# Kernel optimization log

Hardware: AMD Instinct MI355X
Metric: run time of the kernel (lower is better)

## Reference

```python
import jax, jax.numpy as jnp
import numpy as np

HIDDEN = 1024
HEADS = 16
HEAD_DIM = HIDDEN // HEADS
ROPE_BASE = 10000.0


def rope_cos_sin(seq_len, head_dim, dtype=jnp.float32):
    inv_freq = 1.0 / (ROPE_BASE ** (jnp.arange(0, head_dim, 2, dtype=jnp.float32) / head_dim))
    t = jnp.arange(seq_len, dtype=jnp.float32)
    freqs = jnp.einsum('i,j->ij', t, inv_freq)          # [L, head_dim/2]
    emb = jnp.concatenate([freqs, freqs], axis=-1)       # [L, head_dim]
    return emb.astype(dtype), jnp.cos(emb).astype(dtype), jnp.sin(emb).astype(dtype)


def rotate_half(x):
    half = x.shape[-1] // 2
    return jnp.concatenate([-x[..., half:], x[..., :half]], axis=-1)


def setup_inputs() -> dict:
    key = jax.random.key(0)
    kx, kq, kk, kv, ko = jax.random.split(key, 5)
    B, L = 4, 2048
    scale = 1.0 / np.sqrt(HIDDEN)
    x = jax.random.normal(kx, (B, L, HIDDEN), dtype=jnp.float32)
    Wq = jax.random.normal(kq, (HIDDEN, HIDDEN), dtype=jnp.float32) * scale
    Wk = jax.random.normal(kk, (HIDDEN, HIDDEN), dtype=jnp.float32) * scale
    Wv = jax.random.normal(kv, (HIDDEN, HIDDEN), dtype=jnp.float32) * scale
    Wo = jax.random.normal(ko, (HIDDEN, HIDDEN), dtype=jnp.float32) * scale
    return {"x": x, "Wq": Wq, "Wk": Wk, "Wv": Wv, "Wo": Wo}


def reference(x, Wq, Wk, Wv, Wo):
    B, L, D = x.shape
    H, Hd = HEADS, HEAD_DIM
    # projections (nn.Linear: y = x @ W.T; weights here stored already as [out,in])
    q = (x @ Wq.T).reshape(B, L, H, Hd).transpose(0, 2, 1, 3)  # [B,H,L,Hd]
    k = (x @ Wk.T).reshape(B, L, H, Hd).transpose(0, 2, 1, 3)
    v = (x @ Wv.T).reshape(B, L, H, Hd).transpose(0, 2, 1, 3)
    _, cos, sin = rope_cos_sin(L, Hd, x.dtype)                  # [L, Hd]
    cos = cos[None, None, :, :]
    sin = sin[None, None, :, :]
    q = q * cos + rotate_half(q) * sin
    k = k * cos + rotate_half(k) * sin
    scores = jnp.einsum('bhqd,bhkd->bhqk', q, k) / np.sqrt(Hd)  # [B,H,L,L]
    attn = jax.nn.softmax(scores, axis=-1)
    out = jnp.einsum('bhqk,bhkd->bhqd', attn, v)                # [B,H,L,Hd]
    out = out.transpose(0, 2, 1, 3).reshape(B, L, D)
    return out @ Wo.T
```

## Files before the change

### kernel.cpp

```cpp
#include <hip/hip_runtime.h>
#include <math.h>

#define BB 4
#define LL 2048
#define DD 1024
#define HH 16
#define HD 64
#define BL (BB*LL)

typedef __attribute__((ext_vector_type(8))) short bf16x8;
typedef __attribute__((ext_vector_type(4))) short bf16x4;
typedef __attribute__((ext_vector_type(4))) float f32x4;

__device__ inline short f2bf(float f) {
    union { float f; unsigned u; } v; v.f = f;
    unsigned r = v.u + 0x7fffu + ((v.u >> 16) & 1u);
    return (short)(r >> 16);
}

__device__ inline unsigned pk_bf16(float a, float b) {
    union { float f; unsigned u; } x, y; x.f = a; y.f = b;
    return (x.u >> 16) | (y.u & 0xffff0000u);
}

__device__ inline float exp2x(float x) {
#if __has_builtin(__builtin_amdgcn_exp2f)
    return __builtin_amdgcn_exp2f(x);
#else
    return exp2f(x);
#endif
}

__device__ inline void gload_lds16(const void* g, void* l) {
    __builtin_amdgcn_global_load_lds(
        (const __attribute__((address_space(1))) unsigned int*)g,
        (__attribute__((address_space(3))) unsigned int*)l, 16, 0, 0);
}

__global__ __launch_bounds__(256) void cast_kernel(
    const float* __restrict__ in, short* __restrict__ out, int n)
{
    int i = (blockIdx.x * 256 + threadIdx.x) * 8;
    float4 a = *(const float4*)(in + i);
    float4 b = *(const float4*)(in + i + 4);
    bf16x8 o;
    o[0]=f2bf(a.x); o[1]=f2bf(a.y); o[2]=f2bf(a.z); o[3]=f2bf(a.w);
    o[4]=f2bf(b.x); o[5]=f2bf(b.y); o[6]=f2bf(b.z); o[7]=f2bf(b.w);
    *(bf16x8*)(out + i) = o;
}

__global__ __launch_bounds__(256) void cast4_kernel(
    const float* __restrict__ w0, const float* __restrict__ w1,
    const float* __restrict__ w2, const float* __restrict__ w3,
    short* __restrict__ out)
{
    const int nw_blocks = (DD*DD) / 2048;
    int sel = blockIdx.x / nw_blocks;
    int blk = blockIdx.x % nw_blocks;
    const float* in = (sel == 0) ? w0 : (sel == 1) ? w1 : (sel == 2) ? w2 : w3;
    int i = (blk * 256 + threadIdx.x) * 8;
    float4 a = *(const float4*)(in + i);
    float4 b = *(const float4*)(in + i + 4);
    bf16x8 o;
    o[0]=f2bf(a.x); o[1]=f2bf(a.y); o[2]=f2bf(a.z); o[3]=f2bf(a.w);
    o[4]=f2bf(b.x); o[5]=f2bf(b.y); o[6]=f2bf(b.z); o[7]=f2bf(b.w);
    *(bf16x8*)(out + (size_t)sel * DD * DD + i) = o;
}

__global__ __launch_bounds__(256) void rope_tab_kernel(float2* __restrict__ tab)
{
    int idx = blockIdx.x * 256 + threadIdx.x;
    int lq = idx >> 5, f = idx & 31;
    float inv = __expf((float)f * (-9.210340371976184f / 32.0f));
    float s, c;
    sincosf((float)lq * inv, &s, &c);
    tab[idx] = make_float2(c, s);
}

__device__ inline void gemm_bt_128(const short* __restrict__ A,
                                   const short* __restrict__ B,
                                   short* Ash, short* Bsh,
                                   int i0, int n0, f32x4 (&acc)[4][4])
{
    const int t  = threadIdx.x;
    const int w  = t >> 6;
    const int l  = t & 63;
    const int g  = (t >> 4) & 3;
    const int ln = t & 15;
    const int rh = (w >> 1) * 64;
    const int ch = (w & 1) * 64;
    const int srow = w * 8 + (l >> 3);
    const int skol = (l & 7) * 8;

    for (int k0 = 0; k0 < DD; k0 += 64) {
        __syncthreads();
        const short* ga = A + (size_t)(i0 + srow) * DD + k0 + skol;
        const short* gb = B + (size_t)(n0 + srow) * DD + k0 + skol;
        short* la = Ash + w * 512;
        short* lb = Bsh + w * 512;
        #pragma unroll
        for (int j = 0; j < 4; ++j) {
            gload_lds16(ga + j * 32 * DD, la + j * 2048);
            gload_lds16(gb + j * 32 * DD, lb + j * 2048);
        }
        __syncthreads();

        #pragma unroll
        for (int kk = 0; kk < 2; ++kk) {
            bf16x8 af[4], bfr[4];
            #pragma unroll
            for (int mi = 0; mi < 4; ++mi)
                af[mi] = *(const bf16x8*)(Ash + (rh + mi*16 + ln)*64 + kk*32 + 8*g);
            #pragma unroll
            for (int nj = 0; nj < 4; ++nj)
                bfr[nj] = *(const bf16x8*)(Bsh + (ch + nj*16 + ln)*64 + kk*32 + 8*g);
            #pragma unroll
            for (int mi = 0; mi < 4; ++mi)
                #pragma unroll
                for (int nj = 0; nj < 4; ++nj)
                    acc[mi][nj] = __builtin_amdgcn_mfma_f32_16x16x32_bf16(
                        af[mi], bfr[nj], acc[mi][nj], 0, 0, 0);
        }
    }
}

__global__ __launch_bounds__(256) void qkv_mfma_kernel(
    const short* __restrict__ xb, const short* __restrict__ Wqb,
    const short* __restrict__ Wkb, const short* __restrict__ Wvb,
    const float2* __restrict__ rope_tab,
    short* __restrict__ Qo, short* __restrict__ Ko, short* __restrict__ Vo)
{
    __shared__ short Ash[128*64];
    __shared__ short Bsh[128*64];

    const int gid = blockIdx.x;
    const int r8  = gid & 7;
    const int u   = gid >> 3;
    const int i_idx = r8 * 8 + (u & 7);
    const int nz  = u >> 3;
    const int n_idx = nz & 7;
    const int z   = nz >> 3;

    const short* Wm = (z == 0) ? Wqb : ((z == 1) ? Wkb : Wvb);
    const int i0 = i_idx * 128;
    const int n0 = n_idx * 128;

    f32x4 acc[4][4];
    #pragma unroll
    for (int mi = 0; mi < 4; ++mi)
        #pragma unroll
        for (int nj = 0; nj < 4; ++nj) acc[mi][nj] = (f32x4){0.f,0.f,0.f,0.f};

    gemm_bt_128(xb, Wm, Ash, Bsh, i0, n0, acc);

    const int t  = threadIdx.x;
    const int w  = t >> 6;
    const int g  = (t >> 4) & 3;
    const int ln = t & 15;
    const int rh = (w >> 1) * 64;

    if (z == 2) {
        short* buf = Ash;
        const int b = i0 >> 11, l0 = i0 & (LL - 1);
        const int d = t >> 2;
        const int c = t & 3;
        #pragma unroll
        for (int hp = 0; hp < 2; ++hp) {
            __syncthreads();
            if ((w & 1) == hp) {
                #pragma unroll
                for (int nj = 0; nj < 4; ++nj)
                    #pragma unroll
                    for (int mi = 0; mi < 4; ++mi)
                        #pragma unroll
                        for (int r = 0; r < 4; ++r)
                            buf[(nj*16 + ln)*136 + rh + mi*16 + 4*g + r]
                                = f2bf(acc[mi][nj][r]);
            }
            __syncthreads();
            short* dst = Vo + ((size_t)((b*HH + n_idx*2 + hp)*HD + d)) * LL + l0;
            #pragma unroll
            for (int j = 0; j < 4; ++j)
                *(bf16x8*)(dst + c*8 + j*32) =
                    *(const bf16x8*)(buf + d*136 + c*8 + j*32);
        }
    } else {
        const int h = n_idx * 2 + (w & 1);
        short* Om = (z == 0) ? Qo : Ko;
        const float sc = (z == 0) ? 0.180336880111112f : 1.0f;
        #pragma unroll
        for (int mi = 0; mi < 4; ++mi)
            #pragma unroll
            for (int r = 0; r < 4; ++r) {
                int i = i0 + rh + mi*16 + 4*g + r;
                int b = i >> 11, lq = i & (LL - 1);
                float2 cs0 = rope_tab[lq*32 + ln];
                float2 cs1 = rope_tab[lq*32 + ln + 16];
                float r0 = (acc[mi][0][r]*cs0.x - acc[mi][2][r]*cs0.y) * sc;
                float r2 = (acc[mi][2][r]*cs0.x + acc[mi][0][r]*cs0.y) * sc;
                float r1 = (acc[mi][1][r]*cs1.x - acc[mi][3][r]*cs1.y) * sc;
                float r3 = (acc[mi][3][r]*cs1.x + acc[mi][1][r]*cs1.y) * sc;
                size_t base = ((size_t)(b*HH + h) * LL + lq) * HD;
                Om[base + ln     ] = f2bf(r0);
                Om[base + ln + 16] = f2bf(r1);
                Om[base + ln + 32] = f2bf(r2);
                Om[base + ln + 48] = f2bf(r3);
            }
    }
}

__global__ __launch_bounds__(256) void attn_kernel(
    const short* __restrict__ Q, const short* __restrict__ K,
    const short* __restrict__ VT, short* __restrict__ AO)
{
    __shared__ short Ksh[64*72];
    __shared__ short VTs[64*72];

    const int t  = threadIdx.x;
    const int w  = t >> 6;
    const int l  = t & 63;
    const int g  = l >> 4;
    const int ln = l & 15;

    const int bh = blockIdx.x;
    const int q0 = blockIdx.y * 128;
    const short* Qb  = Q  + ((size_t)bh * LL + q0 + w*32) * HD;
    const short* Kb  = K  + (size_t)bh * LL * HD;
    const short* VTb = VT + (size_t)bh * HD * LL;

    bf16x8 qb[2][2];
    #pragma unroll
    for (int qi = 0; qi < 2; ++qi) {
        qb[qi][0] = *(const bf16x8*)(Qb + (size_t)(qi*16 + ln)*HD + 8*g);
        qb[qi][1] = *(const bf16x8*)(Qb + (size_t)(qi*16 + ln)*HD + 32 + 8*g);
    }

    f32x4 O[2][4];
    #pragma unroll
    for (int qi = 0; qi < 2; ++qi)
        #pragma unroll
        for (int db = 0; db < 4; ++db) O[qi][db] = (f32x4){0.f,0.f,0.f,0.f};
    float l_acc[2] = {0.f, 0.f};

    const int sr = t >> 2;
    const int sc = (t & 3) << 4;

    for (int kt = 0; kt < LL; kt += 64) {
        bf16x8 k0 = *(const bf16x8*)(Kb  + (size_t)(kt + sr)*HD + sc);
        bf16x8 k1 = *(const bf16x8*)(Kb  + (size_t)(kt + sr)*HD + sc + 8);
        bf16x8 v0 = *(const bf16x8*)(VTb + (size_t)sr*LL + kt + sc);
        bf16x8 v1 = *(const bf16x8*)(VTb + (size_t)sr*LL + kt + sc + 8);
        __syncthreads();
        *(bf16x8*)(Ksh + sr*72 + sc)     = k0;
        *(bf16x8*)(Ksh + sr*72 + sc + 8) = k1;
        *(bf16x8*)(VTs + sr*72 + sc)     = v0;
        *(bf16x8*)(VTs + sr*72 + sc + 8) = v1;
        __syncthreads();

        unsigned pf[2][4][2];
        #pragma unroll
        for (int kb = 0; kb < 4; ++kb) {
            bf16x8 ka0 = *(const bf16x8*)(Ksh + (kb*16 + ln)*72 + 8*g);
            bf16x8 ka1 = *(const bf16x8*)(Ksh + (kb*16 + ln)*72 + 32 + 8*g);
            #pragma unroll
            for (int qi = 0; qi < 2; ++qi) {
                f32x4 S = (f32x4){0.f,0.f,0.f,0.f};
                S = __builtin_amdgcn_mfma_f32_16x16x32_bf16(ka0, qb[qi][0], S, 0, 0, 0);
                S = __builtin_amdgcn_mfma_f32_16x16x32_bf16(ka1, qb[qi][1], S, 0, 0, 0);
                float p0 = exp2x(S[0]), p1 = exp2x(S[1]);
                float p2 = exp2x(S[2]), p3 = exp2x(S[3]);
                l_acc[qi] += (p0 + p1) + (p2 + p3);
                pf[qi][kb][0] = pk_bf16(p0, p1);
                pf[qi][kb][1] = pk_bf16(p2, p3);
            }
        }

        #pragma unroll
        for (int hb = 0; hb < 2; ++hb) {
            #pragma unroll
            for (int db = 0; db < 4; ++db) {
                const short* vp = VTs + (db*16 + ln)*72 + hb*32 + 4*g;
                bf16x4 vlo = *(const bf16x4*)(vp);
                bf16x4 vhi = *(const bf16x4*)(vp + 16);
                bf16x8 vf = __builtin_shufflevector(vlo, vhi, 0,1,2,3,4,5,6,7);
                #pragma unroll
                for (int qi = 0; qi < 2; ++qi) {
                    union { unsigned u[4]; bf16x8 v; } a;
                    a.u[0] = pf[qi][2*hb][0];   a.u[1] = pf[qi][2*hb][1];
                    a.u[2] = pf[qi][2*hb+1][0]; a.u[3] = pf[qi][2*hb+1][1];
                    O[qi][db] = __builtin_amdgcn_mfma_f32_16x16x32_bf16(
                        a.v, vf, O[qi][db], 0, 0, 0);
                }
            }
        }
    }

    const int b = bh >> 4, h = bh & 15;
    #pragma unroll
    for (int qi = 0; qi < 2; ++qi) {
        float lr = l_acc[qi];
        lr += __shfl_xor(lr, 16);
        lr += __shfl_xor(lr, 32);
        #pragma unroll
        for (int r = 0; r < 4; ++r) {
            float inv = 1.0f / __shfl(lr, 4*g + r);
            int q = q0 + w*32 + qi*16 + 4*g + r;
            size_t base = ((size_t)(b*LL + q)) * DD + h*HD;
            #pragma unroll
            for (int db = 0; db < 4; ++db)
                AO[base + db*16 + ln] = f2bf(O[qi][db][r] * inv);
        }
    }
}

__global__ __launch_bounds__(256) void oproj_mfma_kernel(
    const short* __restrict__ A, const short* __restrict__ Wob,
    float* __restrict__ out)
{
    __shared__ short Ash[128*64];
    __shared__ short Bsh[128*64];

    const int gid = blockIdx.x;
    const int r8  = gid & 7;
    const int u   = gid >> 3;
    const int i_idx = r8 * 8 + (u & 7);
    const int n_idx = u >> 3;
    const int i0 = i_idx * 128;
    const int n0 = n_idx * 128;

    f32x4 acc[4][4];
    #pragma unroll
    for (int mi = 0; mi < 4; ++mi)
        #pragma unroll
        for (int nj = 0; nj < 4; ++nj) acc[mi][nj] = (f32x4){0.f,0.f,0.f,0.f};

    gemm_bt_128(A, Wob, Ash, Bsh, i0, n0, acc);

    const int t  = threadIdx.x;
    const int w  = t >> 6;
    const int g  = (t >> 4) & 3;
    const int ln = t & 15;
    const int rh = (w >> 1) * 64;
    const int ch = (w & 1) * 64;

    #pragma unroll
    for (int mi = 0; mi < 4; ++mi)
        #pragma unroll
        for (int r = 0; r < 4; ++r) {
            size_t base = (size_t)(i0 + rh + mi*16 + 4*g + r) * DD + n0 + ch;
            #pragma unroll
            for (int nj = 0; nj < 4; ++nj)
                out[base + nj*16 + ln] = acc[mi][nj][r];
        }
}

extern "C" void kernel_launch(void* const* d_in, const int* in_sizes, int n_in,
                              void* d_out, int out_size, void* d_ws, size_t ws_size,
                              hipStream_t stream) {
    const float* x  = (const float*)d_in[0];
    const float* Wq = (const float*)d_in[1];
    const float* Wk = (const float*)d_in[2];
    const float* Wv = (const float*)d_in[3];
    const float* Wo = (const float*)d_in[4];
    float* out = (float*)d_out;

    const size_t n_x = (size_t)BL * DD;
    const size_t n_w = (size_t)DD * DD;
    short* xb  = (short*)d_ws;
    short* Wqb = xb  + n_x;
    short* Wkb = Wqb + n_w;
    short* Wvb = Wkb + n_w;
    short* Wob = Wvb + n_w;
    short* Q   = Wob + n_w;
    short* K   = Q   + n_x;
    short* VTg = K   + n_x;
    short* AOb = VTg + n_x;
    float2* tab = (float2*)(AOb + n_x);

    rope_tab_kernel<<<256, 256, 0, stream>>>(tab);
    cast_kernel<<<n_x/2048, 256, 0, stream>>>(x, xb, (int)n_x);
    cast4_kernel<<<4*(n_w/2048), 256, 0, stream>>>(Wq, Wk, Wv, Wo, Wqb);

    qkv_mfma_kernel<<<1536, 256, 0, stream>>>(xb, Wqb, Wkb, Wvb, tab, Q, K, VTg);

    dim3 g2(BB*HH, LL/128);
    attn_kernel<<<g2, 256, 0, stream>>>(Q, K, VTg, AOb);

    oproj_mfma_kernel<<<512, 256, 0, stream>>>(AOb, Wob, out);
}
```

Baseline: 285.7 us.

## Permute V^T layout for single-load B fragments and compute row sums via MFMA

```diff
diff --git a/kernel.cpp b/kernel.cpp
--- a/kernel.cpp
+++ b/kernel.cpp
@@ -20,7 +20,11 @@
 
 __device__ inline unsigned pk_bf16(float a, float b) {
     union { float f; unsigned u; } x, y; x.f = a; y.f = b;
+#if __has_builtin(__builtin_amdgcn_perm)
+    return __builtin_amdgcn_perm(y.u, x.u, 0x07060302u);
+#else
     return (x.u >> 16) | (y.u & 0xffff0000u);
+#endif
 }
 
 __device__ inline float exp2x(float x) {
@@ -180,9 +184,17 @@
             __syncthreads();
             short* dst = Vo + ((size_t)((b*HH + n_idx*2 + hp)*HD + d)) * LL + l0;
             #pragma unroll
-            for (int j = 0; j < 4; ++j)
-                *(bf16x8*)(dst + c*8 + j*32) =
-                    *(const bf16x8*)(buf + d*136 + c*8 + j*32);
+            for (int j = 0; j < 4; ++j) {
+                const short* src = buf + d*136 + c*8 + j*32;
+                bf16x4 lo = *(const bf16x4*)(src);
+                bf16x4 hi = *(const bf16x4*)(src + 4);
+                const int tb = (j >> 1) * 64;
+                const int hb = j & 1;
+                const int aa = c >> 1;
+                const int g0 = (c & 1) * 2;
+                *(bf16x4*)(dst + tb + g0*16       + hb*8 + aa*4) = lo;
+                *(bf16x4*)(dst + tb + (g0+1)*16   + hb*8 + aa*4) = hi;
+            }
         }
     } else {
         const int h = n_idx * 2 + (w & 1);
@@ -235,12 +247,17 @@
         qb[qi][1] = *(const bf16x8*)(Qb + (size_t)(qi*16 + ln)*HD + 32 + 8*g);
     }
 
+    const bf16x8 ONES = { (short)0x3F80, (short)0x3F80, (short)0x3F80, (short)0x3F80,
+                          (short)0x3F80, (short)0x3F80, (short)0x3F80, (short)0x3F80 };
+
     f32x4 O[2][4];
     #pragma unroll
     for (int qi = 0; qi < 2; ++qi)
         #pragma unroll
         for (int db = 0; db < 4; ++db) O[qi][db] = (f32x4){0.f,0.f,0.f,0.f};
-    float l_acc[2] = {0.f, 0.f};
+    f32x4 lsum[2];
+    lsum[0] = (f32x4){0.f,0.f,0.f,0.f};
+    lsum[1] = (f32x4){0.f,0.f,0.f,0.f};
 
     const int sr = t >> 2;
     const int sc = (t & 3) << 4;
@@ -269,28 +286,35 @@
                 S = __builtin_amdgcn_mfma_f32_16x16x32_bf16(ka1, qb[qi][1], S, 0, 0, 0);
                 float p0 = exp2x(S[0]), p1 = exp2x(S[1]);
                 float p2 = exp2x(S[2]), p3 = exp2x(S[3]);
-                l_acc[qi] += (p0 + p1) + (p2 + p3);
                 pf[qi][kb][0] = pk_bf16(p0, p1);
                 pf[qi][kb][1] = pk_bf16(p2, p3);
             }
         }
 
+        bf16x8 pa[2][2];
+        #pragma unroll
+        for (int qi = 0; qi < 2; ++qi)
+            #pragma unroll
+            for (int hb = 0; hb < 2; ++hb) {
+                union { unsigned u[4]; bf16x8 v; } a;
+                a.u[0] = pf[qi][2*hb][0];   a.u[1] = pf[qi][2*hb][1];
+                a.u[2] = pf[qi][2*hb+1][0]; a.u[3] = pf[qi][2*hb+1][1];
+                pa[qi][hb] = a.v;
+            }
+
         #pragma unroll
         for (int hb = 0; hb < 2; ++hb) {
+            lsum[0] = __builtin_amdgcn_mfma_f32_16x16x32_bf16(pa[0][hb], ONES, lsum[0], 0, 0, 0);
+            lsum[1] = __builtin_amdgcn_mfma_f32_16x16x32_bf16(pa[1][hb], ONES, lsum[1], 0, 0, 0);
+        }
+
+        #pragma unroll
+        for (int hb = 0; hb < 2; ++hb) {
             #pragma unroll
             for (int db = 0; db < 4; ++db) {
-                const short* vp = VTs + (db*16 + ln)*72 + hb*32 + 4*g;
-                bf16x4 vlo = *(const bf16x4*)(vp);
-                bf16x4 vhi = *(const bf16x4*)(vp + 16);
-                bf16x8 vf = __builtin_shufflevector(vlo, vhi, 0,1,2,3,4,5,6,7);
-                #pragma unroll
-                for (int qi = 0; qi < 2; ++qi) {
-                    union { unsigned u[4]; bf16x8 v; } a;
-                    a.u[0] = pf[qi][2*hb][0];   a.u[1] = pf[qi][2*hb][1];
-                    a.u[2] = pf[qi][2*hb+1][0]; a.u[3] = pf[qi][2*hb+1][1];
-                    O[qi][db] = __builtin_amdgcn_mfma_f32_16x16x32_bf16(
-                        a.v, vf, O[qi][db], 0, 0, 0);
-                }
+                bf16x8 vf = *(const bf16x8*)(VTs + (db*16 + ln)*72 + 16*g + 8*hb);
+                O[0][db] = __builtin_amdgcn_mfma_f32_16x16x32_bf16(pa[0][hb], vf, O[0][db], 0, 0, 0);
+                O[1][db] = __builtin_amdgcn_mfma_f32_16x16x32_bf16(pa[1][hb], vf, O[1][db], 0, 0, 0);
             }
         }
     }
@@ -298,12 +322,9 @@
     const int b = bh >> 4, h = bh & 15;
     #pragma unroll
     for (int qi = 0; qi < 2; ++qi) {
-        float lr = l_acc[qi];
-        lr += __shfl_xor(lr, 16);
-        lr += __shfl_xor(lr, 32);
         #pragma unroll
         for (int r = 0; r < 4; ++r) {
-            float inv = 1.0f / __shfl(lr, 4*g + r);
+            float inv = 1.0f / lsum[qi][r];
             int q = q0 + w*32 + qi*16 + 4*g + r;
             size_t base = ((size_t)(b*LL + q)) * DD + h*HD;
             #pragma unroll
```

Result: faster. 272.9 us (-4.5%).
